# Optimization experiments

Hardware: AMD Instinct MI355X
Metric: run time of the kernel (lower is better)

The kernel has to match this reference:

```python
import jax, jax.numpy as jnp
import numpy as np
import math

IN_FEATURES = 4096
OUT_FEATURES = 4096
RANK = 16
B, S = 4, 2048


def setup_inputs() -> dict:
    key = jax.random.key(0)
    k_x, k_w, k_b, k_a = jax.random.split(key, 4)
    x = jax.random.normal(k_x, (B, S, IN_FEATURES), dtype=jnp.float32)
    # base linear params (torch nn.Linear default init scale)
    bound_w = 1.0 / math.sqrt(IN_FEATURES)
    W = jax.random.uniform(k_w, (OUT_FEATURES, IN_FEATURES), minval=-bound_w, maxval=bound_w, dtype=jnp.float32)
    bias = jax.random.uniform(k_b, (OUT_FEATURES,), minval=-bound_w, maxval=bound_w, dtype=jnp.float32)
    # lora_A: kaiming_uniform_(a=sqrt(5)) over shape (out, rank) -> fan_in = rank
    bound_a = 1.0 / math.sqrt(RANK)
    lora_A = jax.random.uniform(k_a, (OUT_FEATURES, RANK), minval=-bound_a, maxval=bound_a, dtype=jnp.float32)
    # lora_B initialized to zeros in the module; use small random values so the
    # delta path is numerically exercised in the baseline.
    lora_B = jax.random.normal(jax.random.fold_in(key, 7), (RANK, IN_FEATURES), dtype=jnp.float32) * 0.01
    return {"x": x, "W": W, "bias": bias, "lora_A": lora_A, "lora_B": lora_B}


def reference(x, W, bias, lora_A, lora_B):
    # Faithful to the torch module: materialize the full [out, in] LoRA delta
    # (lora_A @ lora_B), then apply base linear + delta linear.
    lora_update = lora_A @ lora_B                      # [out, in]
    base = jnp.einsum('bsi,oi->bso', x, W) + bias      # base_layer(x)
    delta = jnp.einsum('bsi,oi->bso', x, lora_update)  # F.linear(x, lora_update)
    return base + delta
```

## Files before the change

### kernel.cpp

```cpp
#include <hip/hip_runtime.h>
#include <hip/hip_bf16.h>
#include <stdint.h>


typedef unsigned short u16;
typedef __attribute__((ext_vector_type(8))) u16 u16x8;
typedef __attribute__((ext_vector_type(4))) u16 u16x4;
typedef __attribute__((ext_vector_type(8))) __bf16 bf16x8;
typedef __attribute__((ext_vector_type(4))) float f32x4;

#define IN_F 4096
#define OUT_F 4096
#define MTOT 8192
#define RANK 16
#define NT64 192

__device__ __forceinline__ u16 f2bf(float f) {
  unsigned u = __float_as_uint(f);
  unsigned r = u + 0x7FFFu + ((u >> 16) & 1u);
  return (u16)(r >> 16);
}
__device__ __forceinline__ float bf2f(u16 h) {
  return __uint_as_float(((unsigned)h) << 16);
}

__global__ __launch_bounds__(256) void prep_kernel(
    const float* __restrict__ x, const float* __restrict__ W,
    const float* __restrict__ lA, const float* __restrict__ lB,
    u16* __restrict__ xhi, u16* __restrict__ xlo, u16* __restrict__ whi,
    u16* __restrict__ wlo) {
  if (blockIdx.x < 2048) {
    const int n4 = (MTOT * IN_F) / 4;
    int idx = blockIdx.x * 256 + threadIdx.x;
    for (; idx < n4; idx += 2048 * 256) {
      float4 v = ((const float4*)x)[idx];
      u16x4 h, l;
      h.x = f2bf(v.x); l.x = f2bf(v.x - bf2f(h.x));
      h.y = f2bf(v.y); l.y = f2bf(v.y - bf2f(h.y));
      h.z = f2bf(v.z); l.z = f2bf(v.z - bf2f(h.z));
      h.w = f2bf(v.w); l.w = f2bf(v.w - bf2f(h.w));
      ((u16x4*)xhi)[idx] = h;
      ((u16x4*)xlo)[idx] = l;
    }
  } else {
    const int o = (blockIdx.x - 2048) * 2 + (threadIdx.x >> 7);
    const int tl = threadIdx.x & 127;
    float a[RANK];
#pragma unroll
    for (int r = 0; r < RANK; ++r) a[r] = lA[o * RANK + r];
    const float4* W4 = (const float4*)(W + (size_t)o * IN_F);
    u16x4* h4 = (u16x4*)(whi + (size_t)o * IN_F);
    u16x4* l4 = (u16x4*)(wlo + (size_t)o * IN_F);
    for (int i4 = tl; i4 < IN_F / 4; i4 += 128) {
      float4 acc = W4[i4];
#pragma unroll
      for (int r = 0; r < RANK; ++r) {
        float4 b = ((const float4*)(lB + (size_t)r * IN_F))[i4];
        acc.x += a[r] * b.x; acc.y += a[r] * b.y;
        acc.z += a[r] * b.z; acc.w += a[r] * b.w;
      }
      u16x4 h, l;
      h.x = f2bf(acc.x); l.x = f2bf(acc.x - bf2f(h.x));
      h.y = f2bf(acc.y); l.y = f2bf(acc.y - bf2f(h.y));
      h.z = f2bf(acc.z); l.z = f2bf(acc.z - bf2f(h.z));
      h.w = f2bf(acc.w); l.w = f2bf(acc.w - bf2f(h.w));
      h4[i4] = h; l4[i4] = l;
    }
  }
}

#define GLD_LDS16(g, l)                                                  \
  __builtin_amdgcn_global_load_lds(                                      \
      (const __attribute__((address_space(1))) void*)(g),                \
      (__attribute__((address_space(3))) void*)(l), 16, 0, 0)

__global__ __launch_bounds__(512, 2) void gemm_pipe_kernel(
    const u16* __restrict__ Xhi, const u16* __restrict__ Xlo,
    const u16* __restrict__ Whi, const u16* __restrict__ Wlo,
    const float* __restrict__ bias, float* __restrict__ out) {
  __shared__ __align__(16) u16 LDS[65536];

  const int t = threadIdx.x;
  const int lane = t & 63;
  const int wv = t >> 6;
  const int wm = wv >> 2;
  const int wn = wv & 3;
  const int fr = lane & 15;
  const int fq = lane >> 4;

  const int wg = ((blockIdx.x & 7) << 6) | (blockIdx.x >> 3);
  const int m0 = (wg >> 4) * 256;
  const int n0 = (wg & 15) * 256;

  const int scol = ((t & 7) ^ ((t >> 3) & 7)) * 8;
  const size_t aoff = (size_t)(m0 + (t >> 3)) * IN_F + scol;
  const size_t boff = (size_t)(n0 + (t >> 3)) * IN_F + scol;

  const int lk0 = fr * 64 + (((0 * 4 + fq) ^ (fr & 7)) * 8);
  const int lk1 = fr * 64 + (((1 * 4 + fq) ^ (fr & 7)) * 8);

  f32x4 acc[8][4];
#pragma unroll
  for (int i = 0; i < 8; ++i)
#pragma unroll
    for (int j = 0; j < 4; ++j) {
      acc[i][j][0] = 0.f; acc[i][j][1] = 0.f;
      acc[i][j][2] = 0.f; acc[i][j][3] = 0.f;
    }

  auto stageA = [&](int g, int sbuf) {
    const int sg = g >> 6;
    const u16* ap = (sg == 1) ? Xlo : Xhi;
    const int k0 = (g & 63) << 6;
    u16* dA = (u16*)&LDS[sbuf * 32768];
    const u16* s = ap + aoff + k0;
    GLD_LDS16(s, dA + t * 8);
    GLD_LDS16(s + (size_t)64 * IN_F, dA + (512 + t) * 8);
    GLD_LDS16(s + (size_t)128 * IN_F, dA + (1024 + t) * 8);
    GLD_LDS16(s + (size_t)192 * IN_F, dA + (1536 + t) * 8);
  };
  auto stageB0 = [&](int g, int sbuf) {
    const int sg = g >> 6;
    const u16* bp = (sg == 2) ? Wlo : Whi;
    const int k0 = (g & 63) << 6;
    u16* dB = (u16*)&LDS[sbuf * 32768 + 16384];
    const u16* s = bp + boff + k0;
    GLD_LDS16(s, dB + t * 8);
    GLD_LDS16(s + (size_t)64 * IN_F, dB + (512 + t) * 8);
  };
  auto stageB1 = [&](int g, int sbuf) {
    const int sg = g >> 6;
    const u16* bp = (sg == 2) ? Wlo : Whi;
    const int k0 = (g & 63) << 6;
    u16* dB = (u16*)&LDS[sbuf * 32768 + 16384];
    const u16* s = bp + boff + k0;
    GLD_LDS16(s + (size_t)128 * IN_F, dB + (1024 + t) * 8);
    GLD_LDS16(s + (size_t)192 * IN_F, dB + (1536 + t) * 8);
  };

#define MFMA_Q(AIDX, BARR, BIDX, ACC)                                   \
  ACC = __builtin_amdgcn_mfma_f32_16x16x32_bf16(                        \
      __builtin_bit_cast(bf16x8, af[AIDX]),                             \
      __builtin_bit_cast(bf16x8, BARR[BIDX]), ACC, 0, 0, 0)

  stageA(0, 0); stageB0(0, 0); stageB1(0, 0);

#pragma unroll 1
  for (int tt = 0; tt < NT64; ++tt) {
    const int buf = tt & 1;
    const u16* Ab = &LDS[buf * 32768];
    const u16* Bb = Ab + 16384;
    int g = tt + 1;
    if (g >= NT64) g = NT64 - 1;
    const int sbuf = buf ^ 1;

    asm volatile("s_waitcnt vmcnt(0)" ::: "memory");
    __builtin_amdgcn_s_barrier();
    __builtin_amdgcn_sched_barrier(0);

    u16x8 af[8], bf0[4], bf1[4];

#pragma unroll
    for (int mi = 0; mi < 4; ++mi) {
      af[mi * 2 + 0] = *(const u16x8*)&Ab[wm * 8192 + mi * 1024 + lk0];
      af[mi * 2 + 1] = *(const u16x8*)&Ab[wm * 8192 + mi * 1024 + lk1];
    }
#pragma unroll
    for (int ci = 0; ci < 2; ++ci) {
      bf0[ci * 2 + 0] = *(const u16x8*)&Bb[wn * 4096 + ci * 1024 + lk0];
      bf0[ci * 2 + 1] = *(const u16x8*)&Bb[wn * 4096 + ci * 1024 + lk1];
    }
    stageA(g, sbuf);
    asm volatile("s_waitcnt lgkmcnt(0)" ::: "memory");
    __builtin_amdgcn_sched_barrier(0);
    __builtin_amdgcn_s_setprio(1);
#pragma unroll
    for (int mi = 0; mi < 4; ++mi)
#pragma unroll
      for (int ci = 0; ci < 2; ++ci) {
        MFMA_Q(mi * 2 + 0, bf0, ci * 2 + 0, acc[mi][ci]);
        MFMA_Q(mi * 2 + 1, bf0, ci * 2 + 1, acc[mi][ci]);
      }
    __builtin_amdgcn_s_setprio(0);

#pragma unroll
    for (int ci = 0; ci < 2; ++ci) {
      bf1[ci * 2 + 0] = *(const u16x8*)&Bb[wn * 4096 + 2048 + ci * 1024 + lk0];
      bf1[ci * 2 + 1] = *(const u16x8*)&Bb[wn * 4096 + 2048 + ci * 1024 + lk1];
    }
    stageB0(g, sbuf);
    asm volatile("s_waitcnt lgkmcnt(0)" ::: "memory");
    __builtin_amdgcn_sched_barrier(0);
    __builtin_amdgcn_s_setprio(1);
#pragma unroll
    for (int mi = 0; mi < 4; ++mi)
#pragma unroll
      for (int ci = 0; ci < 2; ++ci) {
        MFMA_Q(mi * 2 + 0, bf1, ci * 2 + 0, acc[mi][2 + ci]);
        MFMA_Q(mi * 2 + 1, bf1, ci * 2 + 1, acc[mi][2 + ci]);
      }
    __builtin_amdgcn_s_setprio(0);

#pragma unroll
    for (int mi = 0; mi < 4; ++mi) {
      af[mi * 2 + 0] = *(const u16x8*)&Ab[wm * 8192 + 4096 + mi * 1024 + lk0];
      af[mi * 2 + 1] = *(const u16x8*)&Ab[wm * 8192 + 4096 + mi * 1024 + lk1];
    }
    stageB1(g, sbuf);
    asm volatile("s_waitcnt lgkmcnt(0)" ::: "memory");
    __builtin_amdgcn_sched_barrier(0);
    __builtin_amdgcn_s_setprio(1);
#pragma unroll
    for (int mi = 0; mi < 4; ++mi)
#pragma unroll
      for (int ci = 0; ci < 2; ++ci) {
        MFMA_Q(mi * 2 + 0, bf1, ci * 2 + 0, acc[4 + mi][2 + ci]);
        MFMA_Q(mi * 2 + 1, bf1, ci * 2 + 1, acc[4 + mi][2 + ci]);
      }
    __builtin_amdgcn_s_setprio(0);

    __builtin_amdgcn_s_setprio(1);
#pragma unroll
    for (int mi = 0; mi < 4; ++mi)
#pragma unroll
      for (int ci = 0; ci < 2; ++ci) {
        MFMA_Q(mi * 2 + 0, bf0, ci * 2 + 0, acc[4 + mi][ci]);
        MFMA_Q(mi * 2 + 1, bf0, ci * 2 + 1, acc[4 + mi][ci]);
      }
    __builtin_amdgcn_s_setprio(0);
  }

#pragma unroll
  for (int a = 0; a < 8; ++a) {
    const int row = m0 + wm * 128 + (a >> 2) * 64 + (a & 3) * 16 + fq * 4;
#pragma unroll
    for (int b = 0; b < 4; ++b) {
      const int col = n0 + wn * 64 + (b >> 1) * 32 + (b & 1) * 16 + fr;
      const float bb = bias[col];
#pragma unroll
      for (int r = 0; r < 4; ++r)
        out[(size_t)(row + r) * OUT_F + col] = acc[a][b][r] + bb;
    }
  }
#undef MFMA_Q
}

__global__ __launch_bounds__(256) void gemm_f32_fallback(
    const float* __restrict__ X, const float* __restrict__ W,
    const float* __restrict__ lA, const float* __restrict__ lB,
    const float* __restrict__ bias, float* __restrict__ out) {
  __shared__ __align__(16) float Xs[64 * 32];
  __shared__ __align__(16) float Ws[64 * 32];
  const int t = threadIdx.x;
  const int bm = blockIdx.x & 127;
  const int bn = blockIdx.x >> 7;
  const int m0 = bm * 64, n0 = bn * 64;
  const int tx = t & 15, ty = t >> 4;
  float acc[4][4] = {};
  for (int k0 = 0; k0 < IN_F; k0 += 32) {
    __syncthreads();
#pragma unroll
    for (int q = 0; q < 2; ++q) {
      const int e4 = t * 2 + q;
      const int row = e4 >> 3;
      const int col = (e4 & 7) * 4;
      float4 xv = *(const float4*)(X + (size_t)(m0 + row) * IN_F + k0 + col);
      *(float4*)(Xs + row * 32 + col) = xv;
      float4 wv = *(const float4*)(W + (size_t)(n0 + row) * IN_F + k0 + col);
#pragma unroll
      for (int r = 0; r < RANK; ++r) {
        const float a = lA[(n0 + row) * RANK + r];
        const float4 b = *(const float4*)(lB + (size_t)r * IN_F + k0 + col);
        wv.x += a * b.x; wv.y += a * b.y; wv.z += a * b.z; wv.w += a * b.w;
      }
      *(float4*)(Ws + row * 32 + col) = wv;
    }
    __syncthreads();
#pragma unroll
    for (int kk = 0; kk < 32; ++kk) {
      float xr[4], wcol[4];
#pragma unroll
      for (int i = 0; i < 4; ++i) xr[i] = Xs[(ty * 4 + i) * 32 + kk];
#pragma unroll
      for (int j = 0; j < 4; ++j) wcol[j] = Ws[(tx * 4 + j) * 32 + kk];
#pragma unroll
      for (int i = 0; i < 4; ++i)
#pragma unroll
        for (int j = 0; j < 4; ++j) acc[i][j] += xr[i] * wcol[j];
    }
  }
#pragma unroll
  for (int i = 0; i < 4; ++i) {
    const int row = m0 + ty * 4 + i;
#pragma unroll
    for (int j = 0; j < 4; ++j) {
      const int col = n0 + tx * 4 + j;
      out[(size_t)row * OUT_F + col] = acc[i][j] + bias[col];
    }
  }
}

extern "C" void kernel_launch(void* const* d_in, const int* in_sizes, int n_in,
                              void* d_out, int out_size, void* d_ws,
                              size_t ws_size, hipStream_t stream) {
  const float* x    = (const float*)d_in[0];
  const float* W    = (const float*)d_in[1];
  const float* bias = (const float*)d_in[2];
  const float* lA   = (const float*)d_in[3];
  const float* lB   = (const float*)d_in[4];
  float* out = (float*)d_out;

  const size_t MK = (size_t)MTOT * IN_F;
  const size_t NK = (size_t)OUT_F * IN_F;
  const size_t need = (MK * 2 + NK * 2) * sizeof(u16);

  if (ws_size >= need) {
    u16* Xhi = (u16*)d_ws;
    u16* Xlo = Xhi + MK;
    u16* Whi = Xlo + MK;
    u16* Wlo = Whi + NK;
    prep_kernel<<<4096, 256, 0, stream>>>(x, W, lA, lB, Xhi, Xlo, Whi, Wlo);
    gemm_pipe_kernel<<<512, 512, 0, stream>>>(Xhi, Xlo, Whi, Wlo, bias, out);
  } else {
    gemm_f32_fallback<<<128 * 64, 256, 0, stream>>>(x, W, lA, lB, bias, out);
  }
}
```

Measured before the change: 910.6 us.

## Restructure LoRA weight-prep reuse and remove per-phase LDS waits in GEMM loop

The prep kernel now keeps each thread's lora_B slice in registers and reuses it across 16 output rows, instead of rereading all 16 lora_B rows for every output row. The split between x-conversion blocks and W-prep blocks also changes. In the GEMM main loop, the A fragments for the second half go into a separate register array, both B halves load up front, the two B staging calls merge into one, and the explicit lgkmcnt(0) waits before each MFMA group are dropped so the compiler can overlap LDS reads with MFMAs. The cost is higher register pressure from the extra af2/bf1 fragments, which could cause spills at launch_bounds(512,2).

```diff
diff --git a/kernel.cpp b/kernel.cpp
--- a/kernel.cpp
+++ b/kernel.cpp
@@ -29,10 +29,11 @@
     const float* __restrict__ lA, const float* __restrict__ lB,
     u16* __restrict__ xhi, u16* __restrict__ xlo, u16* __restrict__ whi,
     u16* __restrict__ wlo) {
-  if (blockIdx.x < 2048) {
+  const int t = threadIdx.x;
+  if (blockIdx.x < 3072) {
     const int n4 = (MTOT * IN_F) / 4;
-    int idx = blockIdx.x * 256 + threadIdx.x;
-    for (; idx < n4; idx += 2048 * 256) {
+    int idx = blockIdx.x * 256 + t;
+    for (; idx < n4; idx += 3072 * 256) {
       float4 v = ((const float4*)x)[idx];
       u16x4 h, l;
       h.x = f2bf(v.x); l.x = f2bf(v.x - bf2f(h.x));
@@ -43,28 +44,37 @@
       ((u16x4*)xlo)[idx] = l;
     }
   } else {
-    const int o = (blockIdx.x - 2048) * 2 + (threadIdx.x >> 7);
-    const int tl = threadIdx.x & 127;
-    float a[RANK];
-#pragma unroll
-    for (int r = 0; r < RANK; ++r) a[r] = lA[o * RANK + r];
-    const float4* W4 = (const float4*)(W + (size_t)o * IN_F);
-    u16x4* h4 = (u16x4*)(whi + (size_t)o * IN_F);
-    u16x4* l4 = (u16x4*)(wlo + (size_t)o * IN_F);
-    for (int i4 = tl; i4 < IN_F / 4; i4 += 128) {
-      float4 acc = W4[i4];
+    const int bw = blockIdx.x - 3072;
+    const int strip = bw & 31;
+    const int og = bw >> 5;
+    const int i4 = strip * 32 + (t & 31);
+    float4 lbr[RANK];
+#pragma unroll
+    for (int r = 0; r < RANK; ++r)
+      lbr[r] = ((const float4*)lB)[r * (IN_F / 4) + i4];
+#pragma unroll 1
+    for (int j = 0; j < 16; ++j) {
+      const int o = og * 128 + (t >> 5) + 8 * j;
+      float a[RANK];
+#pragma unroll
+      for (int q = 0; q < 4; ++q) {
+        float4 av = ((const float4*)lA)[o * (RANK / 4) + q];
+        a[q * 4 + 0] = av.x; a[q * 4 + 1] = av.y;
+        a[q * 4 + 2] = av.z; a[q * 4 + 3] = av.w;
+      }
+      float4 acc = ((const float4*)W)[o * (IN_F / 4) + i4];
 #pragma unroll
       for (int r = 0; r < RANK; ++r) {
-        float4 b = ((const float4*)(lB + (size_t)r * IN_F))[i4];
-        acc.x += a[r] * b.x; acc.y += a[r] * b.y;
-        acc.z += a[r] * b.z; acc.w += a[r] * b.w;
+        acc.x += a[r] * lbr[r].x; acc.y += a[r] * lbr[r].y;
+        acc.z += a[r] * lbr[r].z; acc.w += a[r] * lbr[r].w;
       }
       u16x4 h, l;
       h.x = f2bf(acc.x); l.x = f2bf(acc.x - bf2f(h.x));
       h.y = f2bf(acc.y); l.y = f2bf(acc.y - bf2f(h.y));
       h.z = f2bf(acc.z); l.z = f2bf(acc.z - bf2f(h.z));
       h.w = f2bf(acc.w); l.w = f2bf(acc.w - bf2f(h.w));
-      h4[i4] = h; l4[i4] = l;
+      ((u16x4*)whi)[o * (IN_F / 4) + i4] = h;
+      ((u16x4*)wlo)[o * (IN_F / 4) + i4] = l;
     }
   }
 }
@@ -119,7 +129,7 @@
     GLD_LDS16(s + (size_t)128 * IN_F, dA + (1024 + t) * 8);
     GLD_LDS16(s + (size_t)192 * IN_F, dA + (1536 + t) * 8);
   };
-  auto stageB0 = [&](int g, int sbuf) {
+  auto stageB = [&](int g, int sbuf) {
     const int sg = g >> 6;
     const u16* bp = (sg == 2) ? Wlo : Whi;
     const int k0 = (g & 63) << 6;
@@ -127,23 +137,16 @@
     const u16* s = bp + boff + k0;
     GLD_LDS16(s, dB + t * 8);
     GLD_LDS16(s + (size_t)64 * IN_F, dB + (512 + t) * 8);
-  };
-  auto stageB1 = [&](int g, int sbuf) {
-    const int sg = g >> 6;
-    const u16* bp = (sg == 2) ? Wlo : Whi;
-    const int k0 = (g & 63) << 6;
-    u16* dB = (u16*)&LDS[sbuf * 32768 + 16384];
-    const u16* s = bp + boff + k0;
     GLD_LDS16(s + (size_t)128 * IN_F, dB + (1024 + t) * 8);
     GLD_LDS16(s + (size_t)192 * IN_F, dB + (1536 + t) * 8);
   };
 
-#define MFMA_Q(AIDX, BARR, BIDX, ACC)                                   \
+#define MFMA_Q(AARR, AIDX, BARR, BIDX, ACC)                             \
   ACC = __builtin_amdgcn_mfma_f32_16x16x32_bf16(                        \
-      __builtin_bit_cast(bf16x8, af[AIDX]),                             \
+      __builtin_bit_cast(bf16x8, AARR[AIDX]),                           \
       __builtin_bit_cast(bf16x8, BARR[BIDX]), ACC, 0, 0, 0)
 
-  stageA(0, 0); stageB0(0, 0); stageB1(0, 0);
+  stageA(0, 0); stageB(0, 0);
 
 #pragma unroll 1
   for (int tt = 0; tt < NT64; ++tt) {
@@ -158,7 +161,7 @@
     __builtin_amdgcn_s_barrier();
     __builtin_amdgcn_sched_barrier(0);
 
-    u16x8 af[8], bf0[4], bf1[4];
+    u16x8 af[8], af2[8], bf0[4], bf1[4];
 
 #pragma unroll
     for (int mi = 0; mi < 4; ++mi) {
@@ -169,63 +172,56 @@
     for (int ci = 0; ci < 2; ++ci) {
       bf0[ci * 2 + 0] = *(const u16x8*)&Bb[wn * 4096 + ci * 1024 + lk0];
       bf0[ci * 2 + 1] = *(const u16x8*)&Bb[wn * 4096 + ci * 1024 + lk1];
-    }
-    stageA(g, sbuf);
-    asm volatile("s_waitcnt lgkmcnt(0)" ::: "memory");
-    __builtin_amdgcn_sched_barrier(0);
-    __builtin_amdgcn_s_setprio(1);
-#pragma unroll
-    for (int mi = 0; mi < 4; ++mi)
-#pragma unroll
-      for (int ci = 0; ci < 2; ++ci) {
-        MFMA_Q(mi * 2 + 0, bf0, ci * 2 + 0, acc[mi][ci]);
-        MFMA_Q(mi * 2 + 1, bf0, ci * 2 + 1, acc[mi][ci]);
-      }
-    __builtin_amdgcn_s_setprio(0);
-
-#pragma unroll
-    for (int ci = 0; ci < 2; ++ci) {
       bf1[ci * 2 + 0] = *(const u16x8*)&Bb[wn * 4096 + 2048 + ci * 1024 + lk0];
       bf1[ci * 2 + 1] = *(const u16x8*)&Bb[wn * 4096 + 2048 + ci * 1024 + lk1];
     }
-    stageB0(g, sbuf);
-    asm volatile("s_waitcnt lgkmcnt(0)" ::: "memory");
-    __builtin_amdgcn_sched_barrier(0);
+    stageA(g, sbuf);
+    __builtin_amdgcn_sched_barrier(0);
+
     __builtin_amdgcn_s_setprio(1);
 #pragma unroll
     for (int mi = 0; mi < 4; ++mi)
 #pragma unroll
       for (int ci = 0; ci < 2; ++ci) {
-        MFMA_Q(mi * 2 + 0, bf1, ci * 2 + 0, acc[mi][2 + ci]);
-        MFMA_Q(mi * 2 + 1, bf1, ci * 2 + 1, acc[mi][2 + ci]);
+        MFMA_Q(af, mi * 2 + 0, bf0, ci * 2 + 0, acc[mi][ci]);
+        MFMA_Q(af, mi * 2 + 1, bf0, ci * 2 + 1, acc[mi][ci]);
       }
     __builtin_amdgcn_s_setprio(0);
+    __builtin_amdgcn_sched_barrier(0);
 
 #pragma unroll
     for (int mi = 0; mi < 4; ++mi) {
-      af[mi * 2 + 0] = *(const u16x8*)&Ab[wm * 8192 + 4096 + mi * 1024 + lk0];
-      af[mi * 2 + 1] = *(const u16x8*)&Ab[wm * 8192 + 4096 + mi * 1024 + lk1];
-    }
-    stageB1(g, sbuf);
-    asm volatile("s_waitcnt lgkmcnt(0)" ::: "memory");
-    __builtin_amdgcn_sched_barrier(0);
+      af2[mi * 2 + 0] = *(const u16x8*)&Ab[wm * 8192 + 4096 + mi * 1024 + lk0];
+      af2[mi * 2 + 1] = *(const u16x8*)&Ab[wm * 8192 + 4096 + mi * 1024 + lk1];
+    }
+    stageB(g, sbuf);
+    __builtin_amdgcn_sched_barrier(0);
+
     __builtin_amdgcn_s_setprio(1);
 #pragma unroll
     for (int mi = 0; mi < 4; ++mi)
 #pragma unroll
       for (int ci = 0; ci < 2; ++ci) {
-        MFMA_Q(mi * 2 + 0, bf1, ci * 2 + 0, acc[4 + mi][2 + ci]);
-        MFMA_Q(mi * 2 + 1, bf1, ci * 2 + 1, acc[4 + mi][2 + ci]);
+        MFMA_Q(af, mi * 2 + 0, bf1, ci * 2 + 0, acc[mi][2 + ci]);
+        MFMA_Q(af, mi * 2 + 1, bf1, ci * 2 + 1, acc[mi][2 + ci]);
       }
     __builtin_amdgcn_s_setprio(0);
+    __builtin_amdgcn_sched_barrier(0);
 
     __builtin_amdgcn_s_setprio(1);
 #pragma unroll
     for (int mi = 0; mi < 4; ++mi)
 #pragma unroll
       for (int ci = 0; ci < 2; ++ci) {
-        MFMA_Q(mi * 2 + 0, bf0, ci * 2 + 0, acc[4 + mi][ci]);
-        MFMA_Q(mi * 2 + 1, bf0, ci * 2 + 1, acc[4 + mi][ci]);
+        MFMA_Q(af2, mi * 2 + 0, bf1, ci * 2 + 0, acc[4 + mi][2 + ci]);
+        MFMA_Q(af2, mi * 2 + 1, bf1, ci * 2 + 1, acc[4 + mi][2 + ci]);
+      }
+#pragma unroll
+    for (int mi = 0; mi < 4; ++mi)
+#pragma unroll
+      for (int ci = 0; ci < 2; ++ci) {
+        MFMA_Q(af2, mi * 2 + 0, bf0, ci * 2 + 0, acc[4 + mi][ci]);
+        MFMA_Q(af2, mi * 2 + 1, bf0, ci * 2 + 1, acc[4 + mi][ci]);
       }
     __builtin_amdgcn_s_setprio(0);
   }
```

Result: faster. 883.3 us (-3.0%).
